# Performance work log

Measured on AMD Instinct MI355X. Metric: run time of the kernel, lower is better.

## Reference

```python
import jax, jax.numpy as jnp
import numpy as np

NUM_LEVELS = 4
SEARCH_RADIUS = 4
EPS = 1e-12  # torch F.normalize eps


def _avg_pool2d(x, s):
    # avg pool with kernel=stride=s over last two dims (exact, since H,W divisible by s)
    lead = x.shape[:-2]
    H, W = x.shape[-2], x.shape[-1]
    x = x.reshape(*lead, H // s, s, W // s, s)
    return x.mean(axis=(-3, -1))


def _l2_normalize(x, axis):
    n = jnp.sqrt(jnp.sum(x * x, axis=axis, keepdims=True))
    return x / jnp.maximum(n, EPS)


def _compute_correlation(query, values, radius):
    # query: [B,C,H,W], values: [B,N,C,H,W] -> [B,N,H,W,(2r+1)^2]
    q = _l2_normalize(query, axis=1)
    v = _l2_normalize(values, axis=2)
    corrs = []
    for dy in range(-radius, radius + 1):
        for dx in range(-radius, radius + 1):
            vs = v if (dy == 0 and dx == 0) else jnp.roll(v, (dy, dx), axis=(-2, -1))
            corrs.append(jnp.einsum('bchw,bnchw->bnhw', q, vs))
    return jnp.stack(corrs, axis=-1)


def setup_inputs() -> dict:
    key = jax.random.key(0)
    k1, k2, k3, k4 = jax.random.split(key, 4)
    B, N, C, H, W = 2, 4, 128, 160, 160
    Co = C // 2
    return {
        'query_feat': jax.random.normal(k1, (B, C, H, W), dtype=jnp.float32),
        'value_feats': jax.random.normal(k2, (B, N, C, H, W), dtype=jnp.float32),
        'proj_w': jax.random.normal(k3, (Co, C), dtype=jnp.float32) * (1.0 / np.sqrt(C)),
        'proj_b': jax.random.normal(k4, (Co,), dtype=jnp.float32) * 0.01,
    }


def reference(query_feat, value_feats, proj_w, proj_b):
    # 1x1 conv projection C -> C//2
    q = jnp.einsum('oc,bchw->bohw', proj_w, query_feat) + proj_b[None, :, None, None]
    v = jnp.einsum('oc,bnchw->bnohw', proj_w, value_feats) + proj_b[None, None, :, None, None]
    outs = []
    for level in range(NUM_LEVELS):
        scale = 2 ** level
        radius = max(1, SEARCH_RADIUS // scale)
        if scale > 1:
            q_l = _avg_pool2d(q, scale)
            v_l = _avg_pool2d(v, scale)
        else:
            q_l, v_l = q, v
        outs.append(_compute_correlation(q_l, v_l, radius))
    return tuple(outs)
```

## Files before the change

kernel.cpp:

```cpp
#include <hip/hip_runtime.h>


typedef _Float16 f16;
typedef _Float16 f16x4 __attribute__((ext_vector_type(4)));
typedef _Float16 f16x8 __attribute__((ext_vector_type(8)));
typedef float f32x4 __attribute__((ext_vector_type(4)));

#define EPSN 1e-12f

__global__ __launch_bounds__(256) void prep_weights(
    const float* __restrict__ wt, f16* __restrict__ wh) {
  int gid = blockIdx.x * 256 + threadIdx.x;
  float4 w = *(const float4*)(wt + gid * 4);
  f16x4 h;
  h[0] = (f16)w.x; h[1] = (f16)w.y; h[2] = (f16)w.z; h[3] = (f16)w.w;
  *(f16x4*)(wh + gid * 4) = h;
}

#define LROW 68
#define WS 136

__global__ __launch_bounds__(256, 3) void proj_mfma(
    const float* __restrict__ xq, const float* __restrict__ xv,
    const f16* __restrict__ wh, const float* __restrict__ bias,
    float* __restrict__ outf, f16* __restrict__ outh, int P) {
  __shared__ float xs[128 * LROW];
  __shared__ f16 wsh[64 * WS];

  int bid = blockIdx.x;
  int img = bid / 400;
  int p0 = (bid - img * 400) * 64;
  const float* xsrc = (img < 2) ? (xq + (size_t)img * 128 * P)
                                : (xv + (size_t)(img - 2) * 128 * P);

  int tid = threadIdx.x;
  int lane = tid & 63;
  int wv = tid >> 6;
  int cl = lane & 15;
  int quad = lane >> 4;

  for (int m = tid; m < 1024; m += 256) {
    int o = m >> 4, kk = (m & 15) * 8;
    *(f16x8*)(wsh + o * WS + kk) = *(const f16x8*)(wh + o * 128 + kk);
  }

  {
    int cb = tid >> 4;
    int pxg = (tid & 15) * 4;
#pragma unroll
    for (int i = 0; i < 8; ++i) {
      int c = cb + 16 * i;
      float4 v = *(const float4*)(xsrc + (size_t)c * P + p0 + pxg);
      int x = (pxg + 8 * ((c >> 3) & 3)) & 63;
      *(float4*)(xs + c * LROW + x) = v;
    }
  }
  __syncthreads();

  f32x4 acc[4];
#pragma unroll
  for (int m = 0; m < 4; ++m) acc[m] = (f32x4)0.f;

  int pxl = wv * 16 + cl;
  int xr = (pxl + 8 * quad) & 63;

#pragma unroll
  for (int kc = 0; kc < 4; ++kc) {
    f16x8 bfr;
#pragma unroll
    for (int k = 0; k < 8; ++k) {
      int c = kc * 32 + quad * 8 + k;
      bfr[k] = (f16)xs[c * LROW + xr];
    }
    f16x8 afr[4];
#pragma unroll
    for (int mt = 0; mt < 4; ++mt)
      afr[mt] = *(const f16x8*)(wsh + (mt * 16 + cl) * WS + kc * 32 + quad * 8);
#pragma unroll
    for (int mt = 0; mt < 4; ++mt)
      acc[mt] = __builtin_amdgcn_mfma_f32_16x16x32_f16(afr[mt], bfr, acc[mt], 0, 0, 0);
  }

  float4 bi[4];
#pragma unroll
  for (int mt = 0; mt < 4; ++mt) bi[mt] = *(const float4*)(bias + mt * 16 + quad * 4);

  int px = p0 + pxl;
  float ss = 0.f;
#pragma unroll
  for (int mt = 0; mt < 4; ++mt) {
    acc[mt][0] += bi[mt].x;
    acc[mt][1] += bi[mt].y;
    acc[mt][2] += bi[mt].z;
    acc[mt][3] += bi[mt].w;
#pragma unroll
    for (int r = 0; r < 4; ++r) ss = fmaf(acc[mt][r], acc[mt][r], ss);
  }
  ss += __shfl_xor(ss, 16, 64);
  ss += __shfl_xor(ss, 32, 64);
  float s = 1.0f / fmaxf(sqrtf(ss), EPSN);
  size_t base = ((size_t)img * P + px) * 64;
#pragma unroll
  for (int mt = 0; mt < 4; ++mt) {
    *(float4*)(outf + base + mt * 16 + quad * 4) =
        make_float4(acc[mt][0], acc[mt][1], acc[mt][2], acc[mt][3]);
    f16x4 hn;
    hn[0] = (f16)(acc[mt][0] * s);
    hn[1] = (f16)(acc[mt][1] * s);
    hn[2] = (f16)(acc[mt][2] * s);
    hn[3] = (f16)(acc[mt][3] * s);
    *(f16x4*)(outh + base + mt * 16 + quad * 4) = hn;
  }
}

__global__ __launch_bounds__(256) void pool_all(
    const float* __restrict__ q0, f16* __restrict__ qh1,
    f16* __restrict__ qh2, f16* __restrict__ qh3) {
  int gid = blockIdx.x * 256 + threadIdx.x;
  int c4 = gid & 15;
  int g = (gid >> 4) & 3;
  int idx = gid >> 6;
  int w3 = idx % 20;
  int t = idx / 20;
  int h3 = t % 20;
  int img = t / 20;
  int h2 = 2 * h3 + (g >> 1);
  int w2 = 2 * w3 + (g & 1);

  const float4* in4 = (const float4*)q0;
  size_t base = ((size_t)(img * 160 + 4 * h2) * 160 + 4 * w2) * 16 + c4;
  float4 a[16];
#pragma unroll
  for (int i = 0; i < 4; ++i)
#pragma unroll
    for (int j = 0; j < 4; ++j)
      a[i * 4 + j] = in4[base + (size_t)i * 160 * 16 + j * 16];

  float4 v1[4];
  float4 q2v = make_float4(0.f, 0.f, 0.f, 0.f);
#pragma unroll
  for (int i1 = 0; i1 < 2; ++i1)
#pragma unroll
    for (int j1 = 0; j1 < 2; ++j1) {
      float4 s00 = a[(2 * i1) * 4 + 2 * j1];
      float4 s01 = a[(2 * i1) * 4 + 2 * j1 + 1];
      float4 s10 = a[(2 * i1 + 1) * 4 + 2 * j1];
      float4 s11 = a[(2 * i1 + 1) * 4 + 2 * j1 + 1];
      float4 r;
      r.x = 0.25f * (s00.x + s01.x + s10.x + s11.x);
      r.y = 0.25f * (s00.y + s01.y + s10.y + s11.y);
      r.z = 0.25f * (s00.z + s01.z + s10.z + s11.z);
      r.w = 0.25f * (s00.w + s01.w + s10.w + s11.w);
      v1[i1 * 2 + j1] = r;
      q2v.x += r.x; q2v.y += r.y; q2v.z += r.z; q2v.w += r.w;
    }
  q2v.x *= 0.25f; q2v.y *= 0.25f; q2v.z *= 0.25f; q2v.w *= 0.25f;

#pragma unroll
  for (int i1 = 0; i1 < 2; ++i1)
#pragma unroll
    for (int j1 = 0; j1 < 2; ++j1) {
      float4 r = v1[i1 * 2 + j1];
      float ss = fmaf(r.x, r.x, fmaf(r.y, r.y, fmaf(r.z, r.z, r.w * r.w)));
      ss += __shfl_xor(ss, 1, 64);
      ss += __shfl_xor(ss, 2, 64);
      ss += __shfl_xor(ss, 4, 64);
      ss += __shfl_xor(ss, 8, 64);
      float s = 1.0f / fmaxf(sqrtf(ss), EPSN);
      int y1 = 2 * h2 + i1, x1 = 2 * w2 + j1;
      f16x4 h;
      h[0] = (f16)(r.x * s); h[1] = (f16)(r.y * s);
      h[2] = (f16)(r.z * s); h[3] = (f16)(r.w * s);
      *(f16x4*)(qh1 + ((size_t)(img * 80 + y1) * 80 + x1) * 64 + c4 * 4) = h;
    }

  {
    float ss = fmaf(q2v.x, q2v.x, fmaf(q2v.y, q2v.y, fmaf(q2v.z, q2v.z, q2v.w * q2v.w)));
    ss += __shfl_xor(ss, 1, 64);
    ss += __shfl_xor(ss, 2, 64);
    ss += __shfl_xor(ss, 4, 64);
    ss += __shfl_xor(ss, 8, 64);
    float s = 1.0f / fmaxf(sqrtf(ss), EPSN);
    f16x4 h;
    h[0] = (f16)(q2v.x * s); h[1] = (f16)(q2v.y * s);
    h[2] = (f16)(q2v.z * s); h[3] = (f16)(q2v.w * s);
    *(f16x4*)(qh2 + ((size_t)(img * 40 + h2) * 40 + w2) * 64 + c4 * 4) = h;
  }

  {
    float4 q3v;
    q3v.x = q2v.x + __shfl_xor(q2v.x, 16, 64);
    q3v.y = q2v.y + __shfl_xor(q2v.y, 16, 64);
    q3v.z = q2v.z + __shfl_xor(q2v.z, 16, 64);
    q3v.w = q2v.w + __shfl_xor(q2v.w, 16, 64);
    q3v.x += __shfl_xor(q3v.x, 32, 64);
    q3v.y += __shfl_xor(q3v.y, 32, 64);
    q3v.z += __shfl_xor(q3v.z, 32, 64);
    q3v.w += __shfl_xor(q3v.w, 32, 64);
    q3v.x *= 0.25f; q3v.y *= 0.25f; q3v.z *= 0.25f; q3v.w *= 0.25f;
    float ss = fmaf(q3v.x, q3v.x, fmaf(q3v.y, q3v.y, fmaf(q3v.z, q3v.z, q3v.w * q3v.w)));
    ss += __shfl_xor(ss, 1, 64);
    ss += __shfl_xor(ss, 2, 64);
    ss += __shfl_xor(ss, 4, 64);
    ss += __shfl_xor(ss, 8, 64);
    float s = 1.0f / fmaxf(sqrtf(ss), EPSN);
    if (g == 0) {
      f16x4 h;
      h[0] = (f16)(q3v.x * s); h[1] = (f16)(q3v.y * s);
      h[2] = (f16)(q3v.z * s); h[3] = (f16)(q3v.w * s);
      *(f16x4*)(qh3 + ((size_t)(img * 20 + h3) * 20 + w3) * 64 + c4 * 4) = h;
    }
  }
}

template <int R>
__global__ __launch_bounds__(256, 4) void corr_mfma(
    const f16* __restrict__ qh, const f16* __restrict__ vh,
    float* __restrict__ out, int H, int W, int T) {
  constexpr int D = 2 * R + 1, DD = D * D;
  constexpr int PS = (DD + 3) & ~3;
  __shared__ float lw[4 * 16 * PS];

  int bn = blockIdx.x & 7;
  int wv = threadIdx.x >> 6;
  int widx = (blockIdx.x >> 3) * 4 + wv;
  int h = widx / T;
  int wt = widx - h * T;
  int lane = threadIdx.x & 63;
  int cl = lane & 15, quad = lane >> 4;
  int b = bn >> 2;
  int w0 = wt * 16;
  float* lwv = lw + wv * 16 * PS;

  int ap = w0 + cl; if (ap >= W) ap = W - 1;
  const f16* qp = qh + ((size_t)(b * H + h) * W + ap) * 64 + quad * 8;
  f16x8 a0 = *(const f16x8*)qp;
  f16x8 a1 = *(const f16x8*)(qp + 32);

  int c0 = w0 - R + cl; if (c0 < 0) c0 += W; if (c0 >= W) c0 -= W;
  int c1 = w0 + R + cl; if (c1 >= W) c1 -= W;
  int b0off = c0 * 64 + quad * 8;
  int b1off = c1 * 64 + quad * 8;

  int rbase = quad * 4;
  int base_dxi = rbase - cl + ((quad < 2) ? 2 * R : 0);

  for (int dyi = 0; dyi < D; ++dyi) {
    int h2 = h - dyi + R; if (h2 < 0) h2 += H; else if (h2 >= H) h2 -= H;
    const f16* vrow = vh + ((size_t)(bn * H + h2) * W) * 64;
    f16x8 b0a = *(const f16x8*)(vrow + b0off);
    f16x8 b0b = *(const f16x8*)(vrow + b0off + 32);
    f16x8 b1a = *(const f16x8*)(vrow + b1off);
    f16x8 b1b = *(const f16x8*)(vrow + b1off + 32);
    f32x4 A0 = __builtin_amdgcn_mfma_f32_16x16x32_f16(a0, b0a, (f32x4)0.f, 0, 0, 0);
    A0 = __builtin_amdgcn_mfma_f32_16x16x32_f16(a1, b0b, A0, 0, 0, 0);
    f32x4 A1 = __builtin_amdgcn_mfma_f32_16x16x32_f16(a0, b1a, (f32x4)0.f, 0, 0, 0);
    A1 = __builtin_amdgcn_mfma_f32_16x16x32_f16(a1, b1b, A1, 0, 0, 0);
#pragma unroll
    for (int rr = 0; rr < 4; ++rr) {
      int dxi = base_dxi + rr;
      float val = (quad < 2) ? A0[rr] : A1[rr];
      if ((unsigned)dxi <= (unsigned)(2 * R))
        lwv[(rbase + rr) * PS + dyi * D + dxi] = val;
    }
  }

  int vp = W - w0; if (vp > 16) vp = 16;
  float* ob = out + ((size_t)(bn * H + h) * W + w0) * DD;
  int tot = vp * DD;
  for (int g = lane; g < tot; g += 64) {
    int pl = g / DD;
    int rem = g - pl * DD;
    ob[g] = lwv[pl * PS + rem];
  }
}

extern "C" void kernel_launch(void* const* d_in, const int* in_sizes, int n_in,
                              void* d_out, int out_size, void* d_ws, size_t ws_size,
                              hipStream_t stream) {
  const float* query  = (const float*)d_in[0];
  const float* values = (const float*)d_in[1];
  const float* pw     = (const float*)d_in[2];
  const float* pb     = (const float*)d_in[3];
  float* out = (float*)d_out;
  float* ws  = (float*)d_ws;

  const int B = 2, N = 4;
  const int P0 = 160 * 160;

  float* q0 = ws;
  f16* q0h = (f16*)(ws + (size_t)10 * P0 * 64);
  f16* v0h = q0h + (size_t)2 * P0 * 64;
  f16* qh1 = q0h + (size_t)10 * P0 * 64;
  f16* vh1 = qh1 + (size_t)2 * (P0 / 4) * 64;
  f16* qh2 = vh1 + (size_t)8 * (P0 / 4) * 64;
  f16* vh2 = qh2 + (size_t)2 * (P0 / 16) * 64;
  f16* qh3 = vh2 + (size_t)8 * (P0 / 16) * 64;
  f16* vh3 = qh3 + (size_t)2 * (P0 / 64) * 64;
  f16* wh  = vh3 + (size_t)8 * (P0 / 64) * 64;

  prep_weights<<<8, 256, 0, stream>>>(pw, wh);

  proj_mfma<<<4000, 256, 0, stream>>>(query, values, wh, pb, q0, q0h, P0);

  pool_all<<<1000, 256, 0, stream>>>(q0, qh1, qh2, qh3);

  float* out0 = out;
  float* out1 = out0 + (size_t)B * N * P0 * 81;
  float* out2 = out1 + (size_t)B * N * (P0 / 4) * 25;
  float* out3 = out2 + (size_t)B * N * (P0 / 16) * 9;
  corr_mfma<4><<<8 * 160 * 10 / 4, 256, 0, stream>>>(q0h, v0h, out0, 160, 160, 10);
  corr_mfma<2><<<8 * 80 * 5 / 4, 256, 0, stream>>>(qh1, vh1, out1, 80, 80, 5);
  corr_mfma<1><<<8 * 40 * 3 / 4, 256, 0, stream>>>(qh2, vh2, out2, 40, 40, 3);
  corr_mfma<1><<<8 * 20 * 2 / 4, 256, 0, stream>>>(qh3, vh3, out3, 20, 20, 2);
}
```

Before: 308.6 us.

## Fuse pyramid pooling into projection kernel using 8x8 spatial tiles

The projection kernel now processes 8x8 spatial tiles instead of 64 contiguous pixels. It keeps the fp32 projected tile in shared memory and computes the level 1-3 average pools and normalizations in the same block. This drops the fp32 intermediate buffer write, the separate pool kernel launch, and its global re-read. In exchange it adds shared-memory barriers and uses strided 32-byte row loads for the input tile, which are less coalesced.

After: 307.9 us. About the same (-0.2%).

```diff
diff --git a/kernel.cpp b/kernel.cpp
--- a/kernel.cpp
+++ b/kernel.cpp
@@ -20,16 +20,21 @@
 #define LROW 68
 #define WS 136
 
-__global__ __launch_bounds__(256, 3) void proj_mfma(
+__global__ __launch_bounds__(256, 3) void proj_pool(
     const float* __restrict__ xq, const float* __restrict__ xv,
     const f16* __restrict__ wh, const float* __restrict__ bias,
-    float* __restrict__ outf, f16* __restrict__ outh, int P) {
+    f16* __restrict__ h0, f16* __restrict__ h1,
+    f16* __restrict__ h2, f16* __restrict__ h3, int P) {
   __shared__ float xs[128 * LROW];
   __shared__ f16 wsh[64 * WS];
+  float* accbuf = (float*)wsh;
+  float* l3buf = xs;
 
   int bid = blockIdx.x;
   int img = bid / 400;
-  int p0 = (bid - img * 400) * 64;
+  int t = bid - img * 400;
+  int ty = t / 20, tx = t - ty * 20;
+  int py0 = ty * 8, px0 = tx * 8;
   const float* xsrc = (img < 2) ? (xq + (size_t)img * 128 * P)
                                 : (xv + (size_t)(img - 2) * 128 * P);
 
@@ -46,12 +51,14 @@
 
   {
     int cb = tid >> 4;
-    int pxg = (tid & 15) * 4;
+    int sub = tid & 15;
+    int row = sub >> 1, hf = sub & 1;
 #pragma unroll
     for (int i = 0; i < 8; ++i) {
       int c = cb + 16 * i;
-      float4 v = *(const float4*)(xsrc + (size_t)c * P + p0 + pxg);
-      int x = (pxg + 8 * ((c >> 3) & 3)) & 63;
+      float4 v = *(const float4*)(xsrc + (size_t)c * P + (py0 + row) * 160 + px0 + hf * 4);
+      int p = row * 8 + hf * 4;
+      int x = (p + 8 * ((c >> 3) & 3)) & 63;
       *(float4*)(xs + c * LROW + x) = v;
     }
   }
@@ -85,7 +92,8 @@
 #pragma unroll
   for (int mt = 0; mt < 4; ++mt) bi[mt] = *(const float4*)(bias + mt * 16 + quad * 4);
 
-  int px = p0 + pxl;
+  __syncthreads();
+
   float ss = 0.f;
 #pragma unroll
   for (int mt = 0; mt < 4; ++mt) {
@@ -93,123 +101,105 @@
     acc[mt][1] += bi[mt].y;
     acc[mt][2] += bi[mt].z;
     acc[mt][3] += bi[mt].w;
+    *(float4*)(accbuf + pxl * LROW + mt * 16 + quad * 4) =
+        make_float4(acc[mt][0], acc[mt][1], acc[mt][2], acc[mt][3]);
 #pragma unroll
     for (int r = 0; r < 4; ++r) ss = fmaf(acc[mt][r], acc[mt][r], ss);
   }
   ss += __shfl_xor(ss, 16, 64);
   ss += __shfl_xor(ss, 32, 64);
   float s = 1.0f / fmaxf(sqrtf(ss), EPSN);
-  size_t base = ((size_t)img * P + px) * 64;
-#pragma unroll
-  for (int mt = 0; mt < 4; ++mt) {
-    *(float4*)(outf + base + mt * 16 + quad * 4) =
-        make_float4(acc[mt][0], acc[mt][1], acc[mt][2], acc[mt][3]);
-    f16x4 hn;
-    hn[0] = (f16)(acc[mt][0] * s);
-    hn[1] = (f16)(acc[mt][1] * s);
-    hn[2] = (f16)(acc[mt][2] * s);
-    hn[3] = (f16)(acc[mt][3] * s);
-    *(f16x4*)(outh + base + mt * 16 + quad * 4) = hn;
-  }
-}
-
-__global__ __launch_bounds__(256) void pool_all(
-    const float* __restrict__ q0, f16* __restrict__ qh1,
-    f16* __restrict__ qh2, f16* __restrict__ qh3) {
-  int gid = blockIdx.x * 256 + threadIdx.x;
-  int c4 = gid & 15;
-  int g = (gid >> 4) & 3;
-  int idx = gid >> 6;
-  int w3 = idx % 20;
-  int t = idx / 20;
-  int h3 = t % 20;
-  int img = t / 20;
-  int h2 = 2 * h3 + (g >> 1);
-  int w2 = 2 * w3 + (g & 1);
-
-  const float4* in4 = (const float4*)q0;
-  size_t base = ((size_t)(img * 160 + 4 * h2) * 160 + 4 * w2) * 16 + c4;
-  float4 a[16];
-#pragma unroll
-  for (int i = 0; i < 4; ++i)
-#pragma unroll
-    for (int j = 0; j < 4; ++j)
-      a[i * 4 + j] = in4[base + (size_t)i * 160 * 16 + j * 16];
-
-  float4 v1[4];
-  float4 q2v = make_float4(0.f, 0.f, 0.f, 0.f);
-#pragma unroll
-  for (int i1 = 0; i1 < 2; ++i1)
-#pragma unroll
-    for (int j1 = 0; j1 < 2; ++j1) {
-      float4 s00 = a[(2 * i1) * 4 + 2 * j1];
-      float4 s01 = a[(2 * i1) * 4 + 2 * j1 + 1];
-      float4 s10 = a[(2 * i1 + 1) * 4 + 2 * j1];
-      float4 s11 = a[(2 * i1 + 1) * 4 + 2 * j1 + 1];
-      float4 r;
-      r.x = 0.25f * (s00.x + s01.x + s10.x + s11.x);
-      r.y = 0.25f * (s00.y + s01.y + s10.y + s11.y);
-      r.z = 0.25f * (s00.z + s01.z + s10.z + s11.z);
-      r.w = 0.25f * (s00.w + s01.w + s10.w + s11.w);
-      v1[i1 * 2 + j1] = r;
-      q2v.x += r.x; q2v.y += r.y; q2v.z += r.z; q2v.w += r.w;
-    }
+  {
+    int gp = (py0 + (pxl >> 3)) * 160 + px0 + (pxl & 7);
+    size_t base = ((size_t)img * P + gp) * 64;
+#pragma unroll
+    for (int mt = 0; mt < 4; ++mt) {
+      f16x4 hn;
+      hn[0] = (f16)(acc[mt][0] * s);
+      hn[1] = (f16)(acc[mt][1] * s);
+      hn[2] = (f16)(acc[mt][2] * s);
+      hn[3] = (f16)(acc[mt][3] * s);
+      *(f16x4*)(h0 + base + mt * 16 + quad * 4) = hn;
+    }
+  }
+  __syncthreads();
+
+  int r2 = wv >> 1, c2 = wv & 1;
+  int g = quad, c4 = cl;
+  int r1 = 2 * r2 + (g >> 1), c1 = 2 * c2 + (g & 1);
+  int p00 = (2 * r1) * 8 + 2 * c1;
+
+  float4 s00 = *(const float4*)(accbuf + p00 * LROW + c4 * 4);
+  float4 s01 = *(const float4*)(accbuf + (p00 + 1) * LROW + c4 * 4);
+  float4 s10 = *(const float4*)(accbuf + (p00 + 8) * LROW + c4 * 4);
+  float4 s11 = *(const float4*)(accbuf + (p00 + 9) * LROW + c4 * 4);
+  float4 v1;
+  v1.x = 0.25f * (s00.x + s01.x + s10.x + s11.x);
+  v1.y = 0.25f * (s00.y + s01.y + s10.y + s11.y);
+  v1.z = 0.25f * (s00.z + s01.z + s10.z + s11.z);
+  v1.w = 0.25f * (s00.w + s01.w + s10.w + s11.w);
+
+  {
+    float s1 = fmaf(v1.x, v1.x, fmaf(v1.y, v1.y, fmaf(v1.z, v1.z, v1.w * v1.w)));
+    s1 += __shfl_xor(s1, 1, 64);
+    s1 += __shfl_xor(s1, 2, 64);
+    s1 += __shfl_xor(s1, 4, 64);
+    s1 += __shfl_xor(s1, 8, 64);
+    float sc = 1.0f / fmaxf(sqrtf(s1), EPSN);
+    f16x4 h;
+    h[0] = (f16)(v1.x * sc); h[1] = (f16)(v1.y * sc);
+    h[2] = (f16)(v1.z * sc); h[3] = (f16)(v1.w * sc);
+    *(f16x4*)(h1 + ((size_t)(img * 80 + ty * 4 + r1) * 80 + tx * 4 + c1) * 64 + c4 * 4) = h;
+  }
+
+  float4 q2v;
+  q2v.x = v1.x + __shfl_xor(v1.x, 16, 64);
+  q2v.y = v1.y + __shfl_xor(v1.y, 16, 64);
+  q2v.z = v1.z + __shfl_xor(v1.z, 16, 64);
+  q2v.w = v1.w + __shfl_xor(v1.w, 16, 64);
+  q2v.x += __shfl_xor(q2v.x, 32, 64);
+  q2v.y += __shfl_xor(q2v.y, 32, 64);
+  q2v.z += __shfl_xor(q2v.z, 32, 64);
+  q2v.w += __shfl_xor(q2v.w, 32, 64);
   q2v.x *= 0.25f; q2v.y *= 0.25f; q2v.z *= 0.25f; q2v.w *= 0.25f;
 
-#pragma unroll
-  for (int i1 = 0; i1 < 2; ++i1)
-#pragma unroll
-    for (int j1 = 0; j1 < 2; ++j1) {
-      float4 r = v1[i1 * 2 + j1];
-      float ss = fmaf(r.x, r.x, fmaf(r.y, r.y, fmaf(r.z, r.z, r.w * r.w)));
-      ss += __shfl_xor(ss, 1, 64);
-      ss += __shfl_xor(ss, 2, 64);
-      ss += __shfl_xor(ss, 4, 64);
-      ss += __shfl_xor(ss, 8, 64);
-      float s = 1.0f / fmaxf(sqrtf(ss), EPSN);
-      int y1 = 2 * h2 + i1, x1 = 2 * w2 + j1;
-      f16x4 h;
-      h[0] = (f16)(r.x * s); h[1] = (f16)(r.y * s);
-      h[2] = (f16)(r.z * s); h[3] = (f16)(r.w * s);
-      *(f16x4*)(qh1 + ((size_t)(img * 80 + y1) * 80 + x1) * 64 + c4 * 4) = h;
-    }
-
   {
-    float ss = fmaf(q2v.x, q2v.x, fmaf(q2v.y, q2v.y, fmaf(q2v.z, q2v.z, q2v.w * q2v.w)));
-    ss += __shfl_xor(ss, 1, 64);
-    ss += __shfl_xor(ss, 2, 64);
-    ss += __shfl_xor(ss, 4, 64);
-    ss += __shfl_xor(ss, 8, 64);
-    float s = 1.0f / fmaxf(sqrtf(ss), EPSN);
-    f16x4 h;
-    h[0] = (f16)(q2v.x * s); h[1] = (f16)(q2v.y * s);
-    h[2] = (f16)(q2v.z * s); h[3] = (f16)(q2v.w * s);
-    *(f16x4*)(qh2 + ((size_t)(img * 40 + h2) * 40 + w2) * 64 + c4 * 4) = h;
-  }
-
-  {
-    float4 q3v;
-    q3v.x = q2v.x + __shfl_xor(q2v.x, 16, 64);
-    q3v.y = q2v.y + __shfl_xor(q2v.y, 16, 64);
-    q3v.z = q2v.z + __shfl_xor(q2v.z, 16, 64);
-    q3v.w = q2v.w + __shfl_xor(q2v.w, 16, 64);
-    q3v.x += __shfl_xor(q3v.x, 32, 64);
-    q3v.y += __shfl_xor(q3v.y, 32, 64);
-    q3v.z += __shfl_xor(q3v.z, 32, 64);
-    q3v.w += __shfl_xor(q3v.w, 32, 64);
-    q3v.x *= 0.25f; q3v.y *= 0.25f; q3v.z *= 0.25f; q3v.w *= 0.25f;
-    float ss = fmaf(q3v.x, q3v.x, fmaf(q3v.y, q3v.y, fmaf(q3v.z, q3v.z, q3v.w * q3v.w)));
-    ss += __shfl_xor(ss, 1, 64);
-    ss += __shfl_xor(ss, 2, 64);
-    ss += __shfl_xor(ss, 4, 64);
-    ss += __shfl_xor(ss, 8, 64);
-    float s = 1.0f / fmaxf(sqrtf(ss), EPSN);
+    float s2 = fmaf(q2v.x, q2v.x, fmaf(q2v.y, q2v.y, fmaf(q2v.z, q2v.z, q2v.w * q2v.w)));
+    s2 += __shfl_xor(s2, 1, 64);
+    s2 += __shfl_xor(s2, 2, 64);
+    s2 += __shfl_xor(s2, 4, 64);
+    s2 += __shfl_xor(s2, 8, 64);
+    float sc = 1.0f / fmaxf(sqrtf(s2), EPSN);
     if (g == 0) {
       f16x4 h;
-      h[0] = (f16)(q3v.x * s); h[1] = (f16)(q3v.y * s);
-      h[2] = (f16)(q3v.z * s); h[3] = (f16)(q3v.w * s);
-      *(f16x4*)(qh3 + ((size_t)(img * 20 + h3) * 20 + w3) * 64 + c4 * 4) = h;
-    }
+      h[0] = (f16)(q2v.x * sc); h[1] = (f16)(q2v.y * sc);
+      h[2] = (f16)(q2v.z * sc); h[3] = (f16)(q2v.w * sc);
+      *(f16x4*)(h2 + ((size_t)(img * 40 + ty * 2 + r2) * 40 + tx * 2 + c2) * 64 + c4 * 4) = h;
+      *(float4*)(l3buf + (wv * 16 + c4) * 4) = q2v;
+    }
+  }
+  __syncthreads();
+
+  if (tid < 16) {
+    float4 a0 = *(const float4*)(l3buf + (0 * 16 + tid) * 4);
+    float4 a1 = *(const float4*)(l3buf + (1 * 16 + tid) * 4);
+    float4 a2 = *(const float4*)(l3buf + (2 * 16 + tid) * 4);
+    float4 a3 = *(const float4*)(l3buf + (3 * 16 + tid) * 4);
+    float4 q3;
+    q3.x = 0.25f * (a0.x + a1.x + a2.x + a3.x);
+    q3.y = 0.25f * (a0.y + a1.y + a2.y + a3.y);
+    q3.z = 0.25f * (a0.z + a1.z + a2.z + a3.z);
+    q3.w = 0.25f * (a0.w + a1.w + a2.w + a3.w);
+    float s3 = fmaf(q3.x, q3.x, fmaf(q3.y, q3.y, fmaf(q3.z, q3.z, q3.w * q3.w)));
+    s3 += __shfl_xor(s3, 1, 64);
+    s3 += __shfl_xor(s3, 2, 64);
+    s3 += __shfl_xor(s3, 4, 64);
+    s3 += __shfl_xor(s3, 8, 64);
+    float sc = 1.0f / fmaxf(sqrtf(s3), EPSN);
+    f16x4 h;
+    h[0] = (f16)(q3.x * sc); h[1] = (f16)(q3.y * sc);
+    h[2] = (f16)(q3.z * sc); h[3] = (f16)(q3.w * sc);
+    *(f16x4*)(h3 + ((size_t)(img * 20 + ty) * 20 + tx) * 64 + tid * 4) = h;
   }
 }
 
@@ -268,10 +258,10 @@
   int vp = W - w0; if (vp > 16) vp = 16;
   float* ob = out + ((size_t)(bn * H + h) * W + w0) * DD;
   int tot = vp * DD;
-  for (int g = lane; g < tot; g += 64) {
-    int pl = g / DD;
-    int rem = g - pl * DD;
-    ob[g] = lwv[pl * PS + rem];
+  for (int gg = lane; gg < tot; gg += 64) {
+    int pl = gg / DD;
+    int rem = gg - pl * DD;
+    ob[gg] = lwv[pl * PS + rem];
   }
 }
 
@@ -288,22 +278,20 @@
   const int B = 2, N = 4;
   const int P0 = 160 * 160;
 
-  float* q0 = ws;
-  f16* q0h = (f16*)(ws + (size_t)10 * P0 * 64);
-  f16* v0h = q0h + (size_t)2 * P0 * 64;
-  f16* qh1 = q0h + (size_t)10 * P0 * 64;
-  f16* vh1 = qh1 + (size_t)2 * (P0 / 4) * 64;
-  f16* qh2 = vh1 + (size_t)8 * (P0 / 4) * 64;
-  f16* vh2 = qh2 + (size_t)2 * (P0 / 16) * 64;
-  f16* qh3 = vh2 + (size_t)8 * (P0 / 16) * 64;
-  f16* vh3 = qh3 + (size_t)2 * (P0 / 64) * 64;
-  f16* wh  = vh3 + (size_t)8 * (P0 / 64) * 64;
+  f16* h0 = (f16*)ws;
+  f16* h1 = h0 + (size_t)10 * P0 * 64;
+  f16* h2 = h1 + (size_t)10 * (P0 / 4) * 64;
+  f16* h3 = h2 + (size_t)10 * (P0 / 16) * 64;
+  f16* wh = h3 + (size_t)10 * (P0 / 64) * 64;
+
+  f16* q0h = h0;             f16* v0h = h0 + (size_t)2 * P0 * 64;
+  f16* qh1 = h1;             f16* vh1 = h1 + (size_t)2 * (P0 / 4) * 64;
+  f16* qh2 = h2;             f16* vh2 = h2 + (size_t)2 * (P0 / 16) * 64;
+  f16* qh3 = h3;             f16* vh3 = h3 + (size_t)2 * (P0 / 64) * 64;
 
   prep_weights<<<8, 256, 0, stream>>>(pw, wh);
 
-  proj_mfma<<<4000, 256, 0, stream>>>(query, values, wh, pb, q0, q0h, P0);
-
-  pool_all<<<1000, 256, 0, stream>>>(q0, qh1, qh2, qh3);
+  proj_pool<<<4000, 256, 0, stream>>>(query, values, wh, pb, h0, h1, h2, h3, P0);
 
   float* out0 = out;
   float* out1 = out0 + (size_t)B * N * P0 * 81;
```
